# Optimization experiments

Hardware: AMD Instinct MI355X
Metric: run time of the kernel (lower is better)

The kernel has to match this reference:

```python
import jax, jax.numpy as jnp
import numpy as np

EPS = 1e-06


def setup_inputs() -> dict:
    key = jax.random.key(0)
    k1, k2, k3 = jax.random.split(key, 3)
    L, B, H, D = 4096, 4, 8, 64
    Q = jax.random.normal(k1, (L, B, H, D), dtype=jnp.float32)
    K = jax.random.normal(k2, (L, B, H, D), dtype=jnp.float32)
    V = jax.random.normal(k3, (L, B, H, D), dtype=jnp.float32)
    return {"Q": Q, "K": K, "V": V}


def reference(Q, K, V):
    # feature map: elu(x) + 1 (positive features)
    phiQ = jax.nn.elu(Q) + 1.0  # [L, B, H, D]
    phiK = jax.nn.elu(K) + 1.0  # [L, B, H, D]
    # Associative rewrite of sum_k phiK_k (x) V_k : per-(batch,head) KV state [D, Dv]
    kv = jnp.einsum('lbhd,lbhe->bhde', phiK, V)          # [B, H, D, Dv]
    num = jnp.einsum('lbhd,bhde->lbhe', phiQ, kv)        # [L, B, H, Dv]
    ksum = jnp.sum(phiK, axis=0)                          # [B, H, D]
    den = jnp.einsum('lbhd,bhd->lbh', phiQ, ksum)[..., None]  # [L, B, H, 1]
    return num / (den + EPS)
```

## Files before the change

kernel.cpp:

```cpp
#include <hip/hip_runtime.h>
#include <math.h>


#define L_TOT 4096
#define NBH   32
#define ROWSTRIDE 2048
#define KVSZ  4160
#define EPS_  1e-6f

typedef short s16x8 __attribute__((ext_vector_type(8)));
typedef float f32x4 __attribute__((ext_vector_type(4)));

union FragU { unsigned int u[4]; s16x8 s; };

__device__ __forceinline__ float phi_(float x) {
    return x > 0.0f ? x + 1.0f : __expf(x);
}

__device__ __forceinline__ unsigned int bf16rn_(float x) {
    unsigned int u = __float_as_uint(x);
    return (u + 0x7FFFu + ((u >> 16) & 1u)) >> 16;
}

__device__ __forceinline__ s16x8 frag_from_(const unsigned short* p) {
    uint2 a = *(const uint2*)p;
    uint2 b = *(const uint2*)(p + 4);
    FragU f;
    f.u[0] = a.x; f.u[1] = a.y; f.u[2] = b.x; f.u[3] = b.y;
    return f.s;
}

__global__ __launch_bounds__(256) void kv_partial_kernel(
    const float* __restrict__ K, const float* __restrict__ V,
    float* __restrict__ part, int Lc)
{
    __shared__ __align__(16) unsigned short kphi[64][36];
    __shared__ __align__(16) unsigned short vtr [64][36];

    const int tid  = threadIdx.x;
    const int w    = tid >> 6;
    const int lane = tid & 63;
    const int c    = blockIdx.x;
    const int bh   = blockIdx.y;
    const int l0c  = c * Lc;
    const int ntiles = Lc >> 5;

    const int sr = tid >> 4;
    const int sc = (tid & 15) * 4;
    const size_t bh_off = (size_t)bh * 64;

    const int ar = lane & 15;
    const int ag = lane >> 4;

    f32x4 acc[4];
    f32x4 aks = {0.f, 0.f, 0.f, 0.f};
    #pragma unroll
    for (int n = 0; n < 4; ++n) { f32x4 z = {0.f,0.f,0.f,0.f}; acc[n] = z; }

    FragU onesU;
    #pragma unroll
    for (int p = 0; p < 4; ++p) onesU.u[p] = 0x3F803F80u;
    const s16x8 ones = onesU.s;

    size_t gb = (size_t)(l0c + sr) * ROWSTRIDE + bh_off + sc;
    float4 ka = *(const float4*)(K + gb);
    float4 va = *(const float4*)(V + gb);
    float4 kb = *(const float4*)(K + gb + 16 * ROWSTRIDE);
    float4 vb = *(const float4*)(V + gb + 16 * ROWSTRIDE);

    for (int t = 0; t < ntiles; ++t) {
        {
            float kx[4] = {ka.x, ka.y, ka.z, ka.w};
            float vx[4] = {va.x, va.y, va.z, va.w};
            float ky[4] = {kb.x, kb.y, kb.z, kb.w};
            float vy[4] = {vb.x, vb.y, vb.z, vb.w};
            #pragma unroll
            for (int i = 0; i < 4; ++i) {
                kphi[sc + i][sr]      = (unsigned short)bf16rn_(phi_(kx[i]));
                kphi[sc + i][sr + 16] = (unsigned short)bf16rn_(phi_(ky[i]));
                vtr [sc + i][sr]      = (unsigned short)bf16rn_(vx[i]);
                vtr [sc + i][sr + 16] = (unsigned short)bf16rn_(vy[i]);
            }
        }
        __syncthreads();

        if (t + 1 < ntiles) {
            gb = (size_t)(l0c + (t + 1) * 32 + sr) * ROWSTRIDE + bh_off + sc;
            ka = *(const float4*)(K + gb);
            va = *(const float4*)(V + gb);
            kb = *(const float4*)(K + gb + 16 * ROWSTRIDE);
            vb = *(const float4*)(V + gb + 16 * ROWSTRIDE);
        }

        const s16x8 afrag = frag_from_(&kphi[w * 16 + ar][ag * 8]);

        #pragma unroll
        for (int nt = 0; nt < 4; ++nt) {
            const s16x8 bfrag = frag_from_(&vtr[nt * 16 + ar][ag * 8]);
            acc[nt] = __builtin_amdgcn_mfma_f32_16x16x32_bf16(afrag, bfrag, acc[nt], 0, 0, 0);
        }
        aks = __builtin_amdgcn_mfma_f32_16x16x32_bf16(afrag, ones, aks, 0, 0, 0);

        __syncthreads();
    }

    float* pb = part + ((size_t)c * NBH + bh) * KVSZ;
    #pragma unroll
    for (int nt = 0; nt < 4; ++nt) {
        #pragma unroll
        for (int r = 0; r < 4; ++r) {
            const int d_row = w * 16 + (lane >> 4) * 4 + r;
            const int e_col = nt * 16 + (lane & 15);
            pb[d_row * 64 + e_col] = acc[nt][r];
        }
    }
    if ((lane & 15) == 0) {
        #pragma unroll
        for (int r = 0; r < 4; ++r)
            pb[4096 + w * 16 + (lane >> 4) * 4 + r] = aks[r];
    }
}

__global__ __launch_bounds__(256) void kv_reduce_kernel(
    const float* __restrict__ part, float* __restrict__ fin, int nchunk)
{
    const int i = blockIdx.x * 256 + threadIdx.x;
    if (i >= NBH * KVSZ) return;
    const int bh = i / KVSZ;
    const int r  = i - bh * KVSZ;

    float s = 0.f;
    for (int cc = 0; cc < nchunk; ++cc)
        s += part[((size_t)cc * NBH + bh) * KVSZ + r];

    float* fb = fin + (size_t)bh * KVSZ;
    if (r < 4096) {
        fb[(r & 63) * 64 + (r >> 6)] = s;
    } else {
        fb[r] = s;
    }
}

__global__ __launch_bounds__(256) void attn_out_kernel(
    const float* __restrict__ Q, const float* __restrict__ fin,
    float* __restrict__ out)
{
    __shared__ __align__(16) unsigned short khi[80 * 72];
    __shared__ __align__(16) unsigned short klo[80 * 72];

    const int tid  = threadIdx.x;
    const int lane = tid & 63;
    const int w    = tid >> 6;
    const int bh   = blockIdx.x & 31;
    const int tg   = blockIdx.x >> 5;
    const int wt0  = tg * 128 + w * 32;

    const float* __restrict__ fb = fin + (size_t)bh * KVSZ;

    for (int idx = tid; idx < 2080; idx += 256) {
        const int e = idx >> 5;
        const int p = idx & 31;
        const float2 x2 = *(const float2*)(fb + e * 64 + 2 * p);
        unsigned int u0 = __float_as_uint(x2.x), u1 = __float_as_uint(x2.y);
        unsigned int hi = (u1 & 0xFFFF0000u) | (u0 >> 16);
        float r0 = x2.x - __uint_as_float(u0 & 0xFFFF0000u);
        float r1 = x2.y - __uint_as_float(u1 & 0xFFFF0000u);
        unsigned int lo = (bf16rn_(r1) << 16) | bf16rn_(r0);
        ((unsigned int*)(khi + e * 72))[p] = hi;
        ((unsigned int*)(klo + e * 72))[p] = lo;
    }
    for (int idx = tid; idx < 480; idx += 256) {
        const int e = 65 + (idx >> 5);
        const int p = idx & 31;
        ((unsigned int*)(khi + e * 72))[p] = 0u;
        ((unsigned int*)(klo + e * 72))[p] = 0u;
    }

    const int arow = lane & 15;
    const int agrp = lane >> 4;
    s16x8 ahi[2][2], alo[2][2];
    #pragma unroll
    for (int m = 0; m < 2; ++m) {
        #pragma unroll
        for (int kc = 0; kc < 2; ++kc) {
            const float* qp = Q + (size_t)(wt0 + m*16 + arow) * ROWSTRIDE
                                + (size_t)bh * 64 + kc*32 + agrp*8;
            float4 qa = *(const float4*)qp;
            float4 qb = *(const float4*)(qp + 4);
            float x[8] = {qa.x,qa.y,qa.z,qa.w,qb.x,qb.y,qb.z,qb.w};
            FragU fh, fl;
            #pragma unroll
            for (int p = 0; p < 4; ++p) {
                float p0 = phi_(x[2*p]), p1 = phi_(x[2*p+1]);
                unsigned int u0 = __float_as_uint(p0), u1 = __float_as_uint(p1);
                fh.u[p] = (u1 & 0xFFFF0000u) | (u0 >> 16);
                float r0 = p0 - __uint_as_float(u0 & 0xFFFF0000u);
                float r1 = p1 - __uint_as_float(u1 & 0xFFFF0000u);
                fl.u[p] = (bf16rn_(r1) << 16) | bf16rn_(r0);
            }
            ahi[m][kc] = fh.s;
            alo[m][kc] = fl.s;
        }
    }
    __syncthreads();

    f32x4 acc[2][5];
    #pragma unroll
    for (int m = 0; m < 2; ++m) {
        #pragma unroll
        for (int n = 0; n < 5; ++n) { f32x4 z = {0.f,0.f,0.f,0.f}; acc[m][n] = z; }
    }

    #pragma unroll
    for (int nt = 0; nt < 5; ++nt) {
        #pragma unroll
        for (int kc = 0; kc < 2; ++kc) {
            const int off = (nt*16 + arow) * 72 + kc*32 + agrp*8;
            s16x8 bh_ = *(const s16x8*)(khi + off);
            s16x8 bl_ = *(const s16x8*)(klo + off);
            #pragma unroll
            for (int m = 0; m < 2; ++m) {
                acc[m][nt] = __builtin_amdgcn_mfma_f32_16x16x32_bf16(ahi[m][kc], bh_, acc[m][nt], 0, 0, 0);
                acc[m][nt] = __builtin_amdgcn_mfma_f32_16x16x32_bf16(ahi[m][kc], bl_, acc[m][nt], 0, 0, 0);
                acc[m][nt] = __builtin_amdgcn_mfma_f32_16x16x32_bf16(alo[m][kc], bh_, acc[m][nt], 0, 0, 0);
            }
        }
    }

    const int baddr = (lane & 48) << 2;
    float inv[2][4];
    #pragma unroll
    for (int m = 0; m < 2; ++m) {
        #pragma unroll
        for (int r = 0; r < 4; ++r) {
            float dv = __int_as_float(
                __builtin_amdgcn_ds_bpermute(baddr, __float_as_int(acc[m][4][r])));
            inv[m][r] = 1.0f / (dv + EPS_);
        }
    }

    #pragma unroll
    for (int m = 0; m < 2; ++m) {
        #pragma unroll
        for (int r = 0; r < 4; ++r) {
            const int t = wt0 + m*16 + (lane >> 4) * 4 + r;
            float* op = out + (size_t)t * ROWSTRIDE + (size_t)bh * 64 + (lane & 15);
            #pragma unroll
            for (int nt = 0; nt < 4; ++nt)
                op[nt * 16] = acc[m][nt][r] * inv[m][r];
        }
    }
}

extern "C" void kernel_launch(void* const* d_in, const int* in_sizes, int n_in,
                              void* d_out, int out_size, void* d_ws, size_t ws_size,
                              hipStream_t stream) {
    const float* Q = (const float*)d_in[0];
    const float* K = (const float*)d_in[1];
    const float* V = (const float*)d_in[2];
    float* outp = (float*)d_out;
    float* ws   = (float*)d_ws;

    const size_t slab = (size_t)NBH * KVSZ;
    const size_t cap  = ws_size / (slab * sizeof(float));

    int nchunk = 1;
    {
        const int cand[4] = {16, 8, 4, 2};
        for (int i = 0; i < 4; ++i) {
            if (cap >= (size_t)cand[i] + 1) { nchunk = cand[i]; break; }
        }
    }
    const int Lc = L_TOT / nchunk;

    float* fin  = ws;
    float* part = ws + slab;

    hipLaunchKernelGGL(kv_partial_kernel, dim3(nchunk, NBH), dim3(256), 0, stream,
                       K, V, part, Lc);
    {
        const int nb = (NBH * KVSZ + 255) / 256;
        hipLaunchKernelGGL(kv_reduce_kernel, dim3(nb), dim3(256), 0, stream,
                           part, fin, nchunk);
    }
    hipLaunchKernelGGL(attn_out_kernel, dim3(1024), dim3(256), 0, stream,
                       Q, fin, outp);
}
```

Before: 41.64 us.

## Drop Q low-bf16 split, vectorize KV reduce, use 512-thread output blocks

The output kernel stops splitting phi(Q) into hi/lo bf16 parts and rounds it once to bf16. This removes a third of the MFMAs and the residual conversion work, at the cost of precision on the Q side. The KV reduction now reads float4 chunks and writes four scattered transposed outputs per thread. The output kernel now launches 512 blocks of 512 threads instead of 1024 blocks of 256, so each block covers twice as many rows and the shared K/V conversion is amortised over more rows.

```diff
diff --git a/kernel.cpp b/kernel.cpp
--- a/kernel.cpp
+++ b/kernel.cpp
@@ -124,24 +124,31 @@
 __global__ __launch_bounds__(256) void kv_reduce_kernel(
     const float* __restrict__ part, float* __restrict__ fin, int nchunk)
 {
-    const int i = blockIdx.x * 256 + threadIdx.x;
-    if (i >= NBH * KVSZ) return;
-    const int bh = i / KVSZ;
-    const int r  = i - bh * KVSZ;
-
-    float s = 0.f;
-    for (int cc = 0; cc < nchunk; ++cc)
-        s += part[((size_t)cc * NBH + bh) * KVSZ + r];
-
+    const int i4 = blockIdx.x * 256 + threadIdx.x;
+    if (i4 >= (NBH * KVSZ) / 4) return;
+    const int slab4 = KVSZ / 4;
+    const int bh = i4 / slab4;
+    const int r  = (i4 - bh * slab4) * 4;
+
+    float4 s = make_float4(0.f, 0.f, 0.f, 0.f);
+    for (int cc = 0; cc < nchunk; ++cc) {
+        const float4 v = *(const float4*)(part + ((size_t)cc * NBH + bh) * KVSZ + r);
+        s.x += v.x; s.y += v.y; s.z += v.z; s.w += v.w;
+    }
     float* fb = fin + (size_t)bh * KVSZ;
     if (r < 4096) {
-        fb[(r & 63) * 64 + (r >> 6)] = s;
+        const int d = r >> 6;
+        const int e = r & 63;
+        fb[(e + 0) * 64 + d] = s.x;
+        fb[(e + 1) * 64 + d] = s.y;
+        fb[(e + 2) * 64 + d] = s.z;
+        fb[(e + 3) * 64 + d] = s.w;
     } else {
-        fb[r] = s;
-    }
-}
-
-__global__ __launch_bounds__(256) void attn_out_kernel(
+        fb[r + 0] = s.x; fb[r + 1] = s.y; fb[r + 2] = s.z; fb[r + 3] = s.w;
+    }
+}
+
+__global__ __launch_bounds__(512) void attn_out_kernel(
     const float* __restrict__ Q, const float* __restrict__ fin,
     float* __restrict__ out)
 {
@@ -153,11 +160,11 @@
     const int w    = tid >> 6;
     const int bh   = blockIdx.x & 31;
     const int tg   = blockIdx.x >> 5;
-    const int wt0  = tg * 128 + w * 32;
+    const int wt0  = tg * 256 + w * 32;
 
     const float* __restrict__ fb = fin + (size_t)bh * KVSZ;
 
-    for (int idx = tid; idx < 2080; idx += 256) {
+    for (int idx = tid; idx < 2080; idx += 512) {
         const int e = idx >> 5;
         const int p = idx & 31;
         const float2 x2 = *(const float2*)(fb + e * 64 + 2 * p);
@@ -169,7 +176,7 @@
         ((unsigned int*)(khi + e * 72))[p] = hi;
         ((unsigned int*)(klo + e * 72))[p] = lo;
     }
-    for (int idx = tid; idx < 480; idx += 256) {
+    for (int idx = tid; idx < 480; idx += 512) {
         const int e = 65 + (idx >> 5);
         const int p = idx & 31;
         ((unsigned int*)(khi + e * 72))[p] = 0u;
@@ -178,7 +185,7 @@
 
     const int arow = lane & 15;
     const int agrp = lane >> 4;
-    s16x8 ahi[2][2], alo[2][2];
+    s16x8 ahi[2][2];
     #pragma unroll
     for (int m = 0; m < 2; ++m) {
         #pragma unroll
@@ -188,18 +195,13 @@
             float4 qa = *(const float4*)qp;
             float4 qb = *(const float4*)(qp + 4);
             float x[8] = {qa.x,qa.y,qa.z,qa.w,qb.x,qb.y,qb.z,qb.w};
-            FragU fh, fl;
+            FragU fh;
             #pragma unroll
             for (int p = 0; p < 4; ++p) {
                 float p0 = phi_(x[2*p]), p1 = phi_(x[2*p+1]);
-                unsigned int u0 = __float_as_uint(p0), u1 = __float_as_uint(p1);
-                fh.u[p] = (u1 & 0xFFFF0000u) | (u0 >> 16);
-                float r0 = p0 - __uint_as_float(u0 & 0xFFFF0000u);
-                float r1 = p1 - __uint_as_float(u1 & 0xFFFF0000u);
-                fl.u[p] = (bf16rn_(r1) << 16) | bf16rn_(r0);
+                fh.u[p] = (bf16rn_(p1) << 16) | bf16rn_(p0);
             }
             ahi[m][kc] = fh.s;
-            alo[m][kc] = fl.s;
         }
     }
     __syncthreads();
@@ -222,7 +224,6 @@
             for (int m = 0; m < 2; ++m) {
                 acc[m][nt] = __builtin_amdgcn_mfma_f32_16x16x32_bf16(ahi[m][kc], bh_, acc[m][nt], 0, 0, 0);
                 acc[m][nt] = __builtin_amdgcn_mfma_f32_16x16x32_bf16(ahi[m][kc], bl_, acc[m][nt], 0, 0, 0);
-                acc[m][nt] = __builtin_amdgcn_mfma_f32_16x16x32_bf16(alo[m][kc], bh_, acc[m][nt], 0, 0, 0);
             }
         }
     }
@@ -279,10 +280,10 @@
     hipLaunchKernelGGL(kv_partial_kernel, dim3(nchunk, NBH), dim3(256), 0, stream,
                        K, V, part, Lc);
     {
-        const int nb = (NBH * KVSZ + 255) / 256;
+        const int nb = ((NBH * KVSZ) / 4 + 255) / 256;
         hipLaunchKernelGGL(kv_reduce_kernel, dim3(nb), dim3(256), 0, stream,
                            part, fin, nchunk);
     }
-    hipLaunchKernelGGL(attn_out_kernel, dim3(1024), dim3(256), 0, stream,
+    hipLaunchKernelGGL(attn_out_kernel, dim3(512), dim3(512), 0, stream,
                        Q, fin, outp);
 }
```

Result: faster. 38.44 us (-7.7%).
